# Performance work log

Hardware: AMD Instinct MI355X
Metric: run time of the kernel (lower is better)

The kernel has to match this reference:

```python
import jax, jax.numpy as jnp
import numpy as np

B, S, L, D = 128, 256, 200, 768
POS_VOCAB, POS_DIM = 60, 50
REDUC, HID, TAGS, POL = 400, 150, 5, 4


def setup_inputs() -> dict:
    key = jax.random.key(0)
    ks = jax.random.split(key, 12)
    bert_vectors = jax.random.normal(ks[0], (B, S, D), dtype=jnp.float32)
    # ragged subword spans: word j covers subwords [start_j, end_j] (inclusive), length 1..3,
    # skipping the [CLS] token at index 0. Clipped to S-1 (long sentences just truncate).
    rng = np.random.default_rng(0)
    lens = rng.integers(1, 4, size=(B, L))
    cum = np.cumsum(lens, axis=1)
    starts = 1 + cum - lens
    ends = cum
    starts = np.minimum(starts, S - 1)
    ends = np.minimum(ends, S - 1)
    ends = np.maximum(ends, starts)
    positions = jnp.asarray(np.stack([starts, ends], axis=-1), dtype=jnp.int32)
    postag = jax.random.randint(ks[1], (B, L), 1, POS_VOCAB).astype(jnp.int32)

    def lin(k, o, i):
        return jax.random.normal(k, (o, i), jnp.float32) / np.float32(np.sqrt(i))

    return dict(
        bert_vectors=bert_vectors,
        positions=positions,
        postag=postag,
        embed_table=jax.random.normal(ks[2], (POS_VOCAB, POS_DIM), jnp.float32) * 0.02,
        W_reduc=lin(ks[3], REDUC, D + POS_DIM), b_reduc=jnp.zeros((REDUC,), jnp.float32),
        W_ap=lin(ks[4], HID, REDUC), b_ap=jnp.zeros((HID,), jnp.float32),
        W_op=lin(ks[5], HID, REDUC), b_op=jnp.zeros((HID,), jnp.float32),
        W_ap2=lin(ks[6], HID, REDUC), b_ap2=jnp.zeros((HID,), jnp.float32),
        W_op2=lin(ks[7], HID, REDUC), b_op2=jnp.zeros((HID,), jnp.float32),
        W_aptag=lin(ks[8], TAGS, HID), b_aptag=jnp.zeros((TAGS,), jnp.float32),
        W_optag=lin(ks[9], TAGS, HID), b_optag=jnp.zeros((TAGS,), jnp.float32),
        W_bi=lin(ks[10], POL * HID, HID + 1),
    )


def _pool_subwords(vectors, positions):
    # variable-length mean pooling of subword vectors into word vectors
    # vectors: [B,S,D], positions: [B,L,2] -> [B,L,D]
    idx = jnp.arange(S)[None, None, :]                      # [1,1,S]
    p0 = positions[..., 0][..., None]                       # [B,L,1]
    p1 = positions[..., 1][..., None]
    m = ((idx >= p0) & (idx <= p1)).astype(vectors.dtype)   # [B,L,S]
    cnt = jnp.maximum(m.sum(-1, keepdims=True), 1.0)
    return jnp.einsum('bls,bsd->bld', m, vectors) / cnt


def reference(bert_vectors, positions, postag, embed_table,
              W_reduc, b_reduc, W_ap, b_ap, W_op, b_op,
              W_ap2, b_ap2, W_op2, b_op2,
              W_aptag, b_aptag, W_optag, b_optag, W_bi):
    word_vecs = _pool_subwords(bert_vectors, positions)                 # [B,L,D]
    pos_emb = embed_table[postag]                                       # [B,L,50]
    h = jnp.concatenate([pos_emb, word_vecs], axis=-1)                  # [B,L,D+50]
    reduc = jnp.einsum('blf,of->blo', h, W_reduc) + b_reduc             # [B,L,400]
    ap_rep = jax.nn.relu(jnp.einsum('blf,of->blo', reduc, W_ap) + b_ap)
    op_rep = jax.nn.relu(jnp.einsum('blf,of->blo', reduc, W_op) + b_op)
    ap_node = jax.nn.relu(jnp.einsum('blf,of->blo', reduc, W_ap2) + b_ap2)
    op_node = jax.nn.relu(jnp.einsum('blf,of->blo', reduc, W_op2) + b_op2)
    ap_out = jnp.einsum('blf,of->blo', ap_rep, W_aptag) + b_aptag       # [B,L,5]
    op_out = jnp.einsum('blf,of->blo', op_rep, W_optag) + b_optag       # [B,L,5]
    # Biaffine(150,150,POL,bias=(True,False))
    ones = jnp.ones((B, L, 1), ap_node.dtype)
    in1 = jnp.concatenate([ap_node, ones], axis=-1)                     # [B,L,151]
    affine = jnp.einsum('bli,oi->blo', in1, W_bi).reshape(B, L * POL, HID)
    tri = jnp.einsum('bkh,bmh->bkm', affine, op_node)                   # [B,L*POL,L]
    triplet_out = tri.transpose(0, 2, 1).reshape(B, L, L, POL)          # [B,L2,L1,POL]
    return (ap_out, op_out, triplet_out)
```

## Files before the change

kernel.cpp:

```cpp
#include <hip/hip_runtime.h>
#include <hip/hip_bf16.h>

#define Bsz 128
#define Ssz 256
#define Lsz 200
#define Dsz 768
#define POS_DIM 50
#define TAGS 5
#define NROW 25600
#define FIN 818
#define KH 832
#define KR 416
#define KD 160

typedef __attribute__((ext_vector_type(8))) short short8;
typedef __attribute__((ext_vector_type(4))) short short4v;
typedef __attribute__((ext_vector_type(4))) float floatx4;

__device__ __forceinline__ short f2bf(float v) {
    __hip_bfloat16 h = __float2bfloat16(v);
    short s; __builtin_memcpy(&s, &h, 2); return s;
}
__device__ __forceinline__ float bf2f(short s) {
    __hip_bfloat16 h; __builtin_memcpy(&h, &s, 2);
    return __bfloat162float(h);
}

__device__ __forceinline__ void gload16(const short* g, short* l) {
    __builtin_amdgcn_global_load_lds(
        (const __attribute__((address_space(1))) void*)g,
        (__attribute__((address_space(3))) void*)l, 16, 0, 0);
}

__global__ void prep_kernel(const float* __restrict__ W_reduc,
                            const float* __restrict__ W_ap, const float* __restrict__ W_op,
                            const float* __restrict__ W_ap2, const float* __restrict__ W_op2,
                            const float* __restrict__ W_bi,
                            const float* __restrict__ b_reduc,
                            const float* __restrict__ b_ap, const float* __restrict__ b_op,
                            const float* __restrict__ b_ap2, const float* __restrict__ b_op2,
                            short* __restrict__ Wr_bf, short* __restrict__ Wh_bf,
                            short* __restrict__ Wbi_bf,
                            float* __restrict__ br_pad, float* __restrict__ bh_pad,
                            float* __restrict__ bbi_pad)
{
    int i = blockIdx.x * blockDim.x + threadIdx.x;
    if (i < 512 * KH) {
        int r = i / KH, k = i % KH;
        float v = 0.0f;
        if (r < 400) {
            if (k < 768)       v = W_reduc[r * FIN + POS_DIM + k];
            else if (k < 818)  v = W_reduc[r * FIN + (k - 768)];
        }
        Wr_bf[i] = f2bf(v);
    }
    if (i < 640 * KR) {
        int r = i / KR, c = i % KR;
        float v = 0.0f;
        if (r < 600 && c < 400) {
            const float* src = (r < 150) ? W_ap : (r < 300) ? W_op : (r < 450) ? W_ap2 : W_op2;
            v = src[(r % 150) * 400 + c];
        }
        Wh_bf[i] = f2bf(v);
    }
    if (i < 640 * KD) {
        int r = i / KD, c = i % KD;
        Wbi_bf[i] = (r < 600 && c < 150) ? f2bf(W_bi[r * 151 + c]) : (short)0;
    }
    if (i < KR) br_pad[i] = (i < 400) ? b_reduc[i] : 0.0f;
    if (i < 640) {
        float v = 0.0f;
        if (i < 600) {
            const float* bs = (i < 150) ? b_ap : (i < 300) ? b_op : (i < 450) ? b_ap2 : b_op2;
            v = bs[i % 150];
        }
        bh_pad[i] = v;
        bbi_pad[i] = (i < 600) ? W_bi[i * 151 + 150] : 0.0f;
    }
}

__global__ __launch_bounds__(256) void pool_kernel(
    const float* __restrict__ bert,
    const int* __restrict__ positions,
    const int* __restrict__ postag,
    const float* __restrict__ embed,
    short* __restrict__ h_bf)
{
    int row = blockIdx.x;
    int b = row / Lsz;
    int st = positions[row * 2 + 0];
    int en = positions[row * 2 + 1];
    int tag = postag[row];
    int span = en - st + 1;
    float inv = 1.0f / (float)span;
    const float* base = bert + ((long)b * Ssz + st) * Dsz;
    short* hr = h_bf + (long)row * KH;

    int t = threadIdx.x;
    int c0 = t * 4;
    if (c0 >= KH) return;
    short4v o;
    if (c0 < 768) {
        float4 s = {0.f, 0.f, 0.f, 0.f};
        for (int i = 0; i < span; ++i) {
            float4 v = *(const float4*)(base + i * Dsz + c0);
            s.x += v.x; s.y += v.y; s.z += v.z; s.w += v.w;
        }
        o.x = f2bf(s.x * inv); o.y = f2bf(s.y * inv);
        o.z = f2bf(s.z * inv); o.w = f2bf(s.w * inv);
    } else {
        const float* e = embed + tag * POS_DIM;
#pragma unroll
        for (int j = 0; j < 4; ++j) {
            int c = c0 + j - 768;
            float v = (c < POS_DIM) ? e[c] : 0.0f;
            ((short*)&o)[j] = f2bf(v);
        }
    }
    *(short4v*)(hr + c0) = o;
}

__global__ __launch_bounds__(256) void gemm_mfma(
    const short* __restrict__ A, long long sAb, int lda,
    const short* __restrict__ Bt, long long sBb, int ldb,
    const float* __restrict__ bias,
    short* __restrict__ outB, float* __restrict__ outF, long long sCb, int ldc,
    int M, int Nv, int K, int mode)
{
    __shared__ __align__(16) short AB[6144];

    int bz = blockIdx.z;
    A += (long long)bz * sAb;
    Bt += (long long)bz * sBb;

    int row0 = blockIdx.y * 64;
    int col0 = blockIdx.x * 128;
    int tid = threadIdx.x;
    int lane = tid & 63;
    int wv = tid >> 6;
    int lm = lane & 15, lk = lane >> 4;

    const short* gA0 = A + (long)(row0 + (tid & 63)) * lda + (tid >> 6) * 8;
    int bc0 = tid, bc1 = tid + 256;
    const short* gB0 = Bt + (long)(col0 + (bc0 & 127)) * ldb + (bc0 >> 7) * 8;
    const short* gB1 = Bt + (long)(col0 + (bc1 & 127)) * ldb + (bc1 >> 7) * 8;
    short* lA0 = &AB[tid * 8];
    short* lB0 = &AB[2048 + bc0 * 8];
    short* lB1 = &AB[2048 + bc1 * 8];

    const short* fA = &AB[(lk * 64 + lm) * 8];
    const short* fB = &AB[2048 + (lk * 128 + wv * 32 + lm) * 8];

    floatx4 acc[4][2];
#pragma unroll
    for (int i = 0; i < 4; ++i)
#pragma unroll
        for (int j = 0; j < 2; ++j)
            acc[i][j] = (floatx4){0.f, 0.f, 0.f, 0.f};

    for (int k0 = 0; k0 < K; k0 += 32) {
        gload16(gA0 + k0, lA0);
        gload16(gB0 + k0, lB0);
        gload16(gB1 + k0, lB1);
        __syncthreads();
        short8 a[4], b[2];
#pragma unroll
        for (int mt = 0; mt < 4; ++mt) a[mt] = *(const short8*)(fA + mt * 128);
#pragma unroll
        for (int nt = 0; nt < 2; ++nt) b[nt] = *(const short8*)(fB + nt * 128);
#pragma unroll
        for (int mt = 0; mt < 4; ++mt)
#pragma unroll
            for (int nt = 0; nt < 2; ++nt)
                acc[mt][nt] = __builtin_amdgcn_mfma_f32_16x16x32_bf16(
                    a[mt], b[nt], acc[mt][nt], 0, 0, 0);
        __syncthreads();
    }

#pragma unroll
    for (int mt = 0; mt < 4; ++mt) {
#pragma unroll
        for (int nt = 0; nt < 2; ++nt) {
#pragma unroll
            for (int r = 0; r < 4; ++r) {
                int gm = row0 + mt * 16 + lk * 4 + r;
                int gn = col0 + wv * 32 + nt * 16 + lm;
                float v = acc[mt][nt][r];
                if (mode == 0) {
                    if (gn < Nv)
                        outB[(long)gm * ldc + gn] = f2bf(v + bias[gn]);
                } else if (mode == 1) {
                    if (gn < 600) {
                        v = fmaxf(v + bias[gn], 0.0f);
                        outB[((long)(gn / 150) * NROW + gm) * KD + gn % 150] = f2bf(v);
                    } else if (gn < 640) {
                        int q = gn - 600;
                        outB[((long)(q / 10) * NROW + gm) * KD + 150 + q % 10] = 0;
                    }
                } else if (mode == 2) {
                    int bb = gm / 200, l = gm % 200;
                    if (gn < 600) {
                        v += bias[gn];
                        outB[((long)bb * 800 + l * 4 + gn / 150) * KD + gn % 150] = f2bf(v);
                    } else if (gn < 640) {
                        int q = gn - 600;
                        outB[((long)bb * 800 + l * 4 + q / 10) * KD + 150 + q % 10] = 0;
                    }
                } else {
                    if (gm < M && gn < Nv)
                        outF[(long long)bz * sCb + (long)gm * ldc + gn] = v;
                }
            }
        }
    }
}

__global__ __launch_bounds__(256) void tags_kernel(
    const short* __restrict__ hid4,
    const float* __restrict__ W_aptag, const float* __restrict__ b_aptag,
    const float* __restrict__ W_optag, const float* __restrict__ b_optag,
    float* __restrict__ out_ap, float* __restrict__ out_op)
{
    int wave = threadIdx.x / 64;
    int lane = threadIdx.x % 64;
    int row = blockIdx.x * 4 + wave;
    if (row >= NROW) return;

#pragma unroll
    for (int which = 0; which < 2; ++which) {
        const short* rep = hid4 + ((long)which * NROW + row) * KD;
        const float* W = which ? W_optag : W_aptag;
        const float* bb = which ? b_optag : b_aptag;
        float* out = which ? out_op : out_ap;
        float v0 = bf2f(rep[lane]);
        float v1 = bf2f(rep[64 + lane]);
        float v2 = (lane < 22) ? bf2f(rep[128 + lane]) : 0.0f;
#pragma unroll
        for (int t = 0; t < TAGS; ++t) {
            const float* w = W + t * 150;
            float p = v0 * w[lane] + v1 * w[64 + lane] +
                      ((lane < 22) ? v2 * w[128 + lane] : 0.0f);
#pragma unroll
            for (int off = 32; off > 0; off >>= 1) p += __shfl_down(p, off);
            if (lane == 0) out[row * TAGS + t] = p + bb[t];
        }
    }
}

extern "C" void kernel_launch(void* const* d_in, const int* in_sizes, int n_in,
                              void* d_out, int out_size, void* d_ws, size_t ws_size,
                              hipStream_t stream)
{
    const float* bert      = (const float*)d_in[0];
    const int*   positions = (const int*)d_in[1];
    const int*   postag    = (const int*)d_in[2];
    const float* embed     = (const float*)d_in[3];
    const float* W_reduc   = (const float*)d_in[4];
    const float* b_reduc   = (const float*)d_in[5];
    const float* W_ap      = (const float*)d_in[6];
    const float* b_ap      = (const float*)d_in[7];
    const float* W_op      = (const float*)d_in[8];
    const float* b_op      = (const float*)d_in[9];
    const float* W_ap2     = (const float*)d_in[10];
    const float* b_ap2     = (const float*)d_in[11];
    const float* W_op2     = (const float*)d_in[12];
    const float* b_op2     = (const float*)d_in[13];
    const float* W_aptag   = (const float*)d_in[14];
    const float* b_aptag   = (const float*)d_in[15];
    const float* W_optag   = (const float*)d_in[16];
    const float* b_optag   = (const float*)d_in[17];
    const float* W_bi      = (const float*)d_in[18];

    float* out = (float*)d_out;
    float* out_ap  = out;
    float* out_op  = out + NROW * TAGS;
    float* out_tri = out + 2 * NROW * TAGS;

    short* ws = (short*)d_ws;
    short* h_bf     = ws;
    short* affine   = h_bf;
    short* reduc_bf = h_bf + (long)NROW * KH;
    short* hid4     = reduc_bf + (long)NROW * KR;
    short* Wr_bf    = hid4 + (long)4 * NROW * KD;
    short* Wh_bf    = Wr_bf + 512 * KH;
    short* Wbi_bf   = Wh_bf + 640 * KR;
    float* br_pad   = (float*)(Wbi_bf + 640 * KD);
    float* bh_pad   = br_pad + KR;
    float* bbi_pad  = bh_pad + 640;

    prep_kernel<<<(512 * KH + 255) / 256, 256, 0, stream>>>(
        W_reduc, W_ap, W_op, W_ap2, W_op2, W_bi,
        b_reduc, b_ap, b_op, b_ap2, b_op2,
        Wr_bf, Wh_bf, Wbi_bf, br_pad, bh_pad, bbi_pad);

    pool_kernel<<<NROW, 256, 0, stream>>>(bert, positions, postag, embed, h_bf);

    {
        dim3 g(4, NROW / 64, 1);
        gemm_mfma<<<g, 256, 0, stream>>>(h_bf, 0, KH, Wr_bf, 0, KH, br_pad,
                                         reduc_bf, nullptr, 0, KR,
                                         NROW, KR, KH, 0);
    }
    {
        dim3 g(5, NROW / 64, 1);
        gemm_mfma<<<g, 256, 0, stream>>>(reduc_bf, 0, KR, Wh_bf, 0, KR, bh_pad,
                                         hid4, nullptr, 0, 0,
                                         NROW, 600, KR, 1);
    }
    tags_kernel<<<NROW / 4, 256, 0, stream>>>(hid4, W_aptag, b_aptag,
                                              W_optag, b_optag, out_ap, out_op);
    {
        dim3 g(5, NROW / 64, 1);
        gemm_mfma<<<g, 256, 0, stream>>>(hid4 + (long)2 * NROW * KD, 0, KD,
                                         Wbi_bf, 0, KD, bbi_pad,
                                         affine, nullptr, 0, 0,
                                         NROW, 600, KD, 2);
    }
    {
        dim3 g(7, 4, Bsz);
        gemm_mfma<<<g, 256, 0, stream>>>(hid4 + (long)3 * NROW * KD, (long long)200 * KD, KD,
                                         affine, (long long)800 * KD, KD, nullptr,
                                         nullptr, out_tri, (long long)200 * 800, 800,
                                         200, 800, KD, 3);
    }
}
```

Baseline: 469.8 us.

## Load GEMM fragments directly from global memory with register double buffering

The MFMA GEMM no longer stages A/B tiles through LDS with two barriers per K step. Each wave now loads its bf16 fragments straight from global memory into registers and ping-pongs two register sets so the next tile's loads overlap the current MFMAs. Launch bounds ask for 4 blocks per CU. Every wave now fetches its own A fragments, so A traffic is duplicated across the four waves and relies on cache. The per-lane 16-byte strided loads may also coalesce worse than the LDS-staged path.

```diff
diff --git a/kernel.cpp b/kernel.cpp
--- a/kernel.cpp
+++ b/kernel.cpp
@@ -26,12 +26,6 @@
     return __bfloat162float(h);
 }
 
-__device__ __forceinline__ void gload16(const short* g, short* l) {
-    __builtin_amdgcn_global_load_lds(
-        (const __attribute__((address_space(1))) void*)g,
-        (__attribute__((address_space(3))) void*)l, 16, 0, 0);
-}
-
 __global__ void prep_kernel(const float* __restrict__ W_reduc,
                             const float* __restrict__ W_ap, const float* __restrict__ W_op,
                             const float* __restrict__ W_ap2, const float* __restrict__ W_op2,
@@ -120,36 +114,26 @@
     *(short4v*)(hr + c0) = o;
 }
 
-__global__ __launch_bounds__(256) void gemm_mfma(
+__global__ __launch_bounds__(256, 4) void gemm_mfma(
     const short* __restrict__ A, long long sAb, int lda,
     const short* __restrict__ Bt, long long sBb, int ldb,
     const float* __restrict__ bias,
     short* __restrict__ outB, float* __restrict__ outF, long long sCb, int ldc,
     int M, int Nv, int K, int mode)
 {
-    __shared__ __align__(16) short AB[6144];
-
     int bz = blockIdx.z;
     A += (long long)bz * sAb;
     Bt += (long long)bz * sBb;
 
     int row0 = blockIdx.y * 64;
     int col0 = blockIdx.x * 128;
-    int tid = threadIdx.x;
-    int lane = tid & 63;
-    int wv = tid >> 6;
+    int lane = threadIdx.x & 63;
+    int wv = threadIdx.x >> 6;
     int lm = lane & 15, lk = lane >> 4;
 
-    const short* gA0 = A + (long)(row0 + (tid & 63)) * lda + (tid >> 6) * 8;
-    int bc0 = tid, bc1 = tid + 256;
-    const short* gB0 = Bt + (long)(col0 + (bc0 & 127)) * ldb + (bc0 >> 7) * 8;
-    const short* gB1 = Bt + (long)(col0 + (bc1 & 127)) * ldb + (bc1 >> 7) * 8;
-    short* lA0 = &AB[tid * 8];
-    short* lB0 = &AB[2048 + bc0 * 8];
-    short* lB1 = &AB[2048 + bc1 * 8];
-
-    const short* fA = &AB[(lk * 64 + lm) * 8];
-    const short* fB = &AB[2048 + (lk * 128 + wv * 32 + lm) * 8];
+    const short* pA = A + (long)(row0 + lm) * lda + lk * 8;
+    const short* pB = Bt + (long)(col0 + wv * 32 + lm) * ldb + lk * 8;
+    long ldA16 = (long)lda * 16, ldB16 = (long)ldb * 16;
 
     floatx4 acc[4][2];
 #pragma unroll
@@ -158,24 +142,36 @@
         for (int j = 0; j < 2; ++j)
             acc[i][j] = (floatx4){0.f, 0.f, 0.f, 0.f};
 
-    for (int k0 = 0; k0 < K; k0 += 32) {
-        gload16(gA0 + k0, lA0);
-        gload16(gB0 + k0, lB0);
-        gload16(gB1 + k0, lB1);
-        __syncthreads();
-        short8 a[4], b[2];
-#pragma unroll
-        for (int mt = 0; mt < 4; ++mt) a[mt] = *(const short8*)(fA + mt * 128);
-#pragma unroll
-        for (int nt = 0; nt < 2; ++nt) b[nt] = *(const short8*)(fB + nt * 128);
-#pragma unroll
-        for (int mt = 0; mt < 4; ++mt)
-#pragma unroll
-            for (int nt = 0; nt < 2; ++nt)
-                acc[mt][nt] = __builtin_amdgcn_mfma_f32_16x16x32_bf16(
-                    a[mt], b[nt], acc[mt][nt], 0, 0, 0);
-        __syncthreads();
-    }
+    short8 a0[4], b0[2], a1[4], b1[2];
+
+#define LOADF(k0, aa, bb)                                              \
+    {                                                                  \
+        _Pragma("unroll")                                              \
+        for (int mt = 0; mt < 4; ++mt)                                 \
+            aa[mt] = *(const short8*)(pA + mt * ldA16 + (k0));         \
+        _Pragma("unroll")                                              \
+        for (int nt = 0; nt < 2; ++nt)                                 \
+            bb[nt] = *(const short8*)(pB + nt * ldB16 + (k0));         \
+    }
+#define MFMAF(aa, bb)                                                  \
+    {                                                                  \
+        _Pragma("unroll")                                              \
+        for (int mt = 0; mt < 4; ++mt)                                 \
+            _Pragma("unroll")                                          \
+            for (int nt = 0; nt < 2; ++nt)                             \
+                acc[mt][nt] = __builtin_amdgcn_mfma_f32_16x16x32_bf16( \
+                    aa[mt], bb[nt], acc[mt][nt], 0, 0, 0);             \
+    }
+
+    int niter = K >> 5;
+    LOADF(0, a0, b0);
+    for (int i = 0; i + 1 < niter; i += 2) {
+        LOADF((i + 1) * 32, a1, b1);
+        MFMAF(a0, b0);
+        if (i + 2 < niter) LOADF((i + 2) * 32, a0, b0);
+        MFMAF(a1, b1);
+    }
+    if (niter & 1) MFMAF(a0, b0);
 
 #pragma unroll
     for (int mt = 0; mt < 4; ++mt) {
@@ -213,6 +209,8 @@
             }
         }
     }
+#undef LOADF
+#undef MFMAF
 }
 
 __global__ __launch_bounds__(256) void tags_kernel(
```

After: 508.1 us. 1.08x slower.

## Enlarge MFMA GEMM tile to 256x128 with double-buffered LDS staging

Applied to the files above, without the earlier changes.

Each block of the bf16 MFMA GEMM now computes a 256x128 output tile instead of 64x128. Each wave owns 64 rows across all 128 columns, holding 4x8 accumulators. LDS grows to two 24 KB stages so the next K-slice is loaded while the current one is multiplied, which drops one barrier per iteration. The aim is more operand reuse per LDS load and hiding global-load latency. The costs are higher register and LDS use per block (launch bounds ask for 2 blocks per CU) and fewer blocks in the row-GEMM grids, which can leave CUs underused.

```diff
diff --git a/kernel.cpp b/kernel.cpp
--- a/kernel.cpp
+++ b/kernel.cpp
@@ -120,71 +120,86 @@
     *(short4v*)(hr + c0) = o;
 }
 
-__global__ __launch_bounds__(256) void gemm_mfma(
+__global__ __launch_bounds__(256, 2) void gemm_mfma(
     const short* __restrict__ A, long long sAb, int lda,
     const short* __restrict__ Bt, long long sBb, int ldb,
     const float* __restrict__ bias,
     short* __restrict__ outB, float* __restrict__ outF, long long sCb, int ldc,
     int M, int Nv, int K, int mode)
 {
-    __shared__ __align__(16) short AB[6144];
+    __shared__ __align__(16) short LDSmem[24576];
 
     int bz = blockIdx.z;
     A += (long long)bz * sAb;
     Bt += (long long)bz * sBb;
 
-    int row0 = blockIdx.y * 64;
+    int row0 = blockIdx.y * 256;
     int col0 = blockIdx.x * 128;
     int tid = threadIdx.x;
     int lane = tid & 63;
     int wv = tid >> 6;
     int lm = lane & 15, lk = lane >> 4;
 
-    const short* gA0 = A + (long)(row0 + (tid & 63)) * lda + (tid >> 6) * 8;
-    int bc0 = tid, bc1 = tid + 256;
-    const short* gB0 = Bt + (long)(col0 + (bc0 & 127)) * ldb + (bc0 >> 7) * 8;
-    const short* gB1 = Bt + (long)(col0 + (bc1 & 127)) * ldb + (bc1 >> 7) * 8;
-    short* lA0 = &AB[tid * 8];
-    short* lB0 = &AB[2048 + bc0 * 8];
-    short* lB1 = &AB[2048 + bc1 * 8];
-
-    const short* fA = &AB[(lk * 64 + lm) * 8];
-    const short* fB = &AB[2048 + (lk * 128 + wv * 32 + lm) * 8];
-
-    floatx4 acc[4][2];
+    const short* gA[4];
+#pragma unroll
+    for (int c = 0; c < 4; ++c)
+        gA[c] = A + (long)(row0 + tid) * lda + c * 8;
+    const short* gB[2];
+#pragma unroll
+    for (int c = 0; c < 2; ++c) {
+        int s = c * 256 + tid;
+        gB[c] = Bt + (long)(col0 + (s & 127)) * ldb + (s >> 7) * 8;
+    }
+
+#define STAGE(k0, p)                                                     \
+    {                                                                    \
+        short* lb = &LDSmem[(p) * 12288];                                \
+        _Pragma("unroll")                                                \
+        for (int c = 0; c < 4; ++c)                                      \
+            gload16(gA[c] + (k0), lb + (c * 256 + tid) * 8);             \
+        _Pragma("unroll")                                                \
+        for (int c = 0; c < 2; ++c)                                      \
+            gload16(gB[c] + (k0), lb + 8192 + (c * 256 + tid) * 8);      \
+    }
+
+    floatx4 acc[4][8];
 #pragma unroll
     for (int i = 0; i < 4; ++i)
 #pragma unroll
-        for (int j = 0; j < 2; ++j)
+        for (int j = 0; j < 8; ++j)
             acc[i][j] = (floatx4){0.f, 0.f, 0.f, 0.f};
 
-    for (int k0 = 0; k0 < K; k0 += 32) {
-        gload16(gA0 + k0, lA0);
-        gload16(gB0 + k0, lB0);
-        gload16(gB1 + k0, lB1);
+    int niter = K >> 5;
+    STAGE(0, 0);
+    int p = 0;
+    for (int i = 0; i < niter; ++i) {
         __syncthreads();
-        short8 a[4], b[2];
+        if (i + 1 < niter) STAGE((i + 1) * 32, p ^ 1);
+        const short* fA = &LDSmem[p * 12288 + (lk * 256 + wv * 64 + lm) * 8];
+        const short* fB = &LDSmem[p * 12288 + 8192 + (lk * 128 + lm) * 8];
+        short8 a[4], b[8];
 #pragma unroll
         for (int mt = 0; mt < 4; ++mt) a[mt] = *(const short8*)(fA + mt * 128);
 #pragma unroll
-        for (int nt = 0; nt < 2; ++nt) b[nt] = *(const short8*)(fB + nt * 128);
+        for (int nt = 0; nt < 8; ++nt) b[nt] = *(const short8*)(fB + nt * 128);
 #pragma unroll
         for (int mt = 0; mt < 4; ++mt)
 #pragma unroll
-            for (int nt = 0; nt < 2; ++nt)
+            for (int nt = 0; nt < 8; ++nt)
                 acc[mt][nt] = __builtin_amdgcn_mfma_f32_16x16x32_bf16(
                     a[mt], b[nt], acc[mt][nt], 0, 0, 0);
-        __syncthreads();
-    }
+        p ^= 1;
+    }
+#undef STAGE
 
 #pragma unroll
     for (int mt = 0; mt < 4; ++mt) {
 #pragma unroll
-        for (int nt = 0; nt < 2; ++nt) {
+        for (int nt = 0; nt < 8; ++nt) {
 #pragma unroll
             for (int r = 0; r < 4; ++r) {
-                int gm = row0 + mt * 16 + lk * 4 + r;
-                int gn = col0 + wv * 32 + nt * 16 + lm;
+                int gm = row0 + wv * 64 + mt * 16 + lk * 4 + r;
+                int gn = col0 + nt * 16 + lm;
                 float v = acc[mt][nt][r];
                 if (mode == 0) {
                     if (gn < Nv)
@@ -296,13 +311,13 @@
     pool_kernel<<<NROW, 256, 0, stream>>>(bert, positions, postag, embed, h_bf);
 
     {
-        dim3 g(4, NROW / 64, 1);
+        dim3 g(4, NROW / 256, 1);
         gemm_mfma<<<g, 256, 0, stream>>>(h_bf, 0, KH, Wr_bf, 0, KH, br_pad,
                                          reduc_bf, nullptr, 0, KR,
                                          NROW, KR, KH, 0);
     }
     {
-        dim3 g(5, NROW / 64, 1);
+        dim3 g(5, NROW / 256, 1);
         gemm_mfma<<<g, 256, 0, stream>>>(reduc_bf, 0, KR, Wh_bf, 0, KR, bh_pad,
                                          hid4, nullptr, 0, 0,
                                          NROW, 600, KR, 1);
@@ -310,14 +325,14 @@
     tags_kernel<<<NROW / 4, 256, 0, stream>>>(hid4, W_aptag, b_aptag,
                                               W_optag, b_optag, out_ap, out_op);
     {
-        dim3 g(5, NROW / 64, 1);
+        dim3 g(5, NROW / 256, 1);
         gemm_mfma<<<g, 256, 0, stream>>>(hid4 + (long)2 * NROW * KD, 0, KD,
                                          Wbi_bf, 0, KD, bbi_pad,
                                          affine, nullptr, 0, 0,
                                          NROW, 600, KD, 2);
     }
     {
-        dim3 g(7, 4, Bsz);
+        dim3 g(7, 1, Bsz);
         gemm_mfma<<<g, 256, 0, stream>>>(hid4 + (long)3 * NROW * KD, (long long)200 * KD, KD,
                                          affine, (long long)800 * KD, KD, nullptr,
                                          nullptr, out_tri, (long long)200 * 800, 800,
```

New measurement: 1.050 ms. 2.23x slower.
